# Kernel tuning notes

Hardware: AMD Instinct MI355X
Metric: run time of the kernel (lower is better)

## Reference

```python
import jax, jax.numpy as jnp
import numpy as np


def setup_inputs() -> dict:
    key = jax.random.key(0)
    k1, k2, k3, k4, k5 = jax.random.split(key, 5)
    B, S, D_IN, D_OUT = 4, 2048, 4096, 4096
    inp = jax.random.normal(k1, (B, S, D_IN), dtype=jnp.float32)
    w_q = jax.random.randint(k2, (D_OUT, D_IN), 0, 255, dtype=jnp.int32)
    scale = jax.random.uniform(k3, (D_OUT, 1), dtype=jnp.float32) * 0.02 + 1e-3
    zero_point = jax.random.randint(k4, (D_OUT, 1), 0, 255, dtype=jnp.int32)
    bias = jax.random.normal(k5, (D_OUT,), dtype=jnp.float32)
    return {"input": inp, "w_q": w_q, "scale": scale, "zero_point": zero_point, "bias": bias}


def reference(input, w_q, scale, zero_point, bias):
    # decompress_module: dequantize int weight with per-output-channel affine params
    # W[o, i] = (w_q[o, i] - zp[o]) * scale[o]   -> full fp32 weight materialized
    W = (w_q - zero_point).astype(jnp.float32) * scale  # [D_OUT, D_IN]
    # F.linear: y = x @ W^T + b
    return jnp.einsum("bsi,oi->bso", input, W) + bias
```

## Files before the change

kernel.cpp:

```cpp
#include <hip/hip_runtime.h>
#include <hip/hip_bf16.h>
#include <stdint.h>

typedef float  f32x4  __attribute__((ext_vector_type(4)));
typedef float  f32x16 __attribute__((ext_vector_type(16)));
typedef unsigned int   u32x4 __attribute__((ext_vector_type(4)));
typedef unsigned short u16x4 __attribute__((ext_vector_type(4)));
typedef int    i32x4  __attribute__((ext_vector_type(4)));

__device__ inline unsigned short f2bf(float f) {
  unsigned int u = __builtin_bit_cast(unsigned int, f);
  u += 0x7fffu + ((u >> 16) & 1u);
  return (unsigned short)(u >> 16);
}

__device__ inline void mfma32x32x16bf16(f32x16& acc, u32x4 a, u32x4 b) {
  asm volatile("v_mfma_f32_32x32x16_bf16 %0, %1, %2, %0"
               : "+v"(acc)
               : "v"(a), "v"(b));
}

__device__ inline void mfma16x16x32bf16(f32x4& acc, u32x4 a, u32x4 b) {
  asm volatile("v_mfma_f32_16x16x32_bf16 %0, %1, %2, %0"
               : "+v"(acc)
               : "v"(a), "v"(b));
}

__device__ inline void gload16(const unsigned short* src, char* ldsdst) {
  __builtin_amdgcn_global_load_lds(
      (const __attribute__((address_space(1))) void*)src,
      (__attribute__((address_space(3))) void*)ldsdst, 16, 0, 0);
}


__global__ __launch_bounds__(256) void prep_x(const float* __restrict__ x,
                                              unsigned short* __restrict__ xb,
                                              int K, int KT) {
  const int rb = blockIdx.x / KT;
  const int kt = blockIdx.x % KT;
  __shared__ unsigned short t[256 * 64];
  const int tid = threadIdx.x;
  const int klane = tid & 15;
  const int rbase = tid >> 4;
  const float* src = x + (size_t)(rb * 256) * K + kt * 64;
  const int gw = klane >> 1, hw = klane & 1;
  for (int it = 0; it < 16; ++it) {
    int row = it * 16 + rbase;
    f32x4 v = *(const f32x4*)(src + (size_t)row * K + klane * 4);
    u16x4 h;
    h[0] = f2bf(v[0]); h[1] = f2bf(v[1]); h[2] = f2bf(v[2]); h[3] = f2bf(v[3]);
    *(u16x4*)&t[row * 64 + ((gw ^ (row & 7)) << 3) + hw * 4] = h;
  }
  __syncthreads();
  unsigned short* dst = xb + ((size_t)rb * KT + kt) * 16384;
  for (int j = 0; j < 8; ++j) {
    int c = j * 256 + tid;
    int l = c & 63, f = (c >> 6) & 7, s = c >> 9;
    int row = f * 32 + (l & 31);
    int g   = (s * 2 + (l >> 5)) ^ (row & 7);
    u32x4 v = *(const u32x4*)&t[row * 64 + (g << 3)];
    *(u32x4*)(dst + (size_t)c * 8) = v;
  }
}

__global__ __launch_bounds__(256) void prep_w(const int* __restrict__ wq,
                                              const int* __restrict__ zp,
                                              unsigned short* __restrict__ wb,
                                              int K, int KT) {
  const int cb = blockIdx.x / KT;
  const int kt = blockIdx.x % KT;
  __shared__ unsigned short t[256 * 64];
  const int tid = threadIdx.x;
  const int klane = tid & 15;
  const int rbase = tid >> 4;
  const int* src = wq + (size_t)(cb * 256) * K + kt * 64;
  const int gw = klane >> 1, hw = klane & 1;
  for (int it = 0; it < 16; ++it) {
    int row = it * 16 + rbase;
    i32x4 v = *(const i32x4*)(src + (size_t)row * K + klane * 4);
    int z = zp[cb * 256 + row];
    u16x4 h;
    h[0] = f2bf((float)(v[0] - z)); h[1] = f2bf((float)(v[1] - z));
    h[2] = f2bf((float)(v[2] - z)); h[3] = f2bf((float)(v[3] - z));
    *(u16x4*)&t[row * 64 + ((gw ^ (row & 7)) << 3) + hw * 4] = h;
  }
  __syncthreads();
  unsigned short* dst = wb + ((size_t)cb * KT + kt) * 16384;
  for (int j = 0; j < 8; ++j) {
    int c = j * 256 + tid;
    int l = c & 63, f = (c >> 6) & 7, s = c >> 9;
    int row = f * 32 + (l & 31);
    int g   = (s * 2 + (l >> 5)) ^ (row & 7);
    u32x4 v = *(const u32x4*)&t[row * 64 + (g << 3)];
    *(u32x4*)(dst + (size_t)c * 8) = v;
  }
}

__global__ __launch_bounds__(512, 2) void gemm_ring(
    const unsigned short* __restrict__ xb, const unsigned short* __restrict__ wb,
    const float* __restrict__ scale, const float* __restrict__ bias,
    float* __restrict__ out, int N, int KT) {

  __shared__ unsigned short lds[65536];

  const int NB = N >> 8;
  const int nwg = gridDim.x;
  const int wg  = (blockIdx.x & 7) * (nwg >> 3) + (blockIdx.x >> 3);
  const int rb = wg / NB;
  const int cb = wg % NB;

  const int tid  = threadIdx.x;
  const int lane = tid & 63;
  const int wave = tid >> 6;
  const int wr = wave >> 2;
  const int wc = wave & 3;
  const int wr4 = wr * 4, wc2 = wc * 2;
  const int lane16 = lane * 16;

  const unsigned short* xtb = xb + (size_t)rb * (KT >> 1) * 16384;
  const unsigned short* wtb = wb + (size_t)cb * (KT >> 1) * 16384;

  f32x16 acc[4][2] = {};

  auto STAGE = [&](int u) {
    const int slot = (u & 3) << 15;
    const unsigned short* as = xtb + (size_t)u * 8192;
    const unsigned short* bs = wtb + (size_t)u * 8192;
    char* da = (char*)lds + slot + wave * 2048;
    char* db = (char*)lds + slot + 16384 + wave * 2048;
    gload16(as + wave * 1024 + lane * 8, da);
    gload16(as + wave * 1024 + 512 + lane * 8, da + 1024);
    gload16(bs + wave * 1024 + lane * 8, db);
    gload16(bs + wave * 1024 + 512 + lane * 8, db + 1024);
  };

  auto LDA = [&](int slotb, int s, int m) -> u32x4 {
    return *(const u32x4*)((const char*)lds + slotb + s * 8192 +
                           (wr4 + m) * 1024 + lane16);
  };
  auto LDB = [&](int slotb, int s, int n) -> u32x4 {
    return *(const u32x4*)((const char*)lds + slotb + 16384 + s * 8192 +
                           (wc2 + n) * 1024 + lane16);
  };

#define BODY(U, VM, ST)                                                        \
  {                                                                            \
    const int u_ = (U);                                                        \
    const int sb = (u_ & 3) << 15;                                             \
    asm volatile("s_waitcnt vmcnt(" #VM ")" ::: "memory");                     \
    __builtin_amdgcn_s_barrier();    \
                              \
    {                                                                          \
      u32x4 b0 = LDB(sb, 0, 0), b1 = LDB(sb, 0, 1);                            \
      u32x4 a0 = LDA(sb, 0, 0), a1 = LDA(sb, 0, 1);                            \
      u32x4 a2 = LDA(sb, 0, 2), a3 = LDA(sb, 0, 3);                            \
      if (ST) STAGE(u_ + 3);                                                   \
      asm volatile("s_waitcnt lgkmcnt(0)" ::: "memory");                       \
      __builtin_amdgcn_s_setprio(1);                                           \
      mfma32x32x16bf16(acc[0][0], a0, b0);                                     \
      mfma32x32x16bf16(acc[0][1], a0, b1);                                     \
      mfma32x32x16bf16(acc[1][0], a1, b0);                                     \
      mfma32x32x16bf16(acc[1][1], a1, b1);                                     \
      mfma32x32x16bf16(acc[2][0], a2, b0);                                     \
      mfma32x32x16bf16(acc[2][1], a2, b1);                                     \
      mfma32x32x16bf16(acc[3][0], a3, b0);                                     \
      mfma32x32x16bf16(acc[3][1], a3, b1);                                     \
      __builtin_amdgcn_s_setprio(0);                                           \
    }                                                                          \
    __builtin_amdgcn_s_barrier();                      \
                              \
    {                                                                          \
      u32x4 b0 = LDB(sb, 1, 0), b1 = LDB(sb, 1, 1);                            \
      u32x4 a0 = LDA(sb, 1, 0), a1 = LDA(sb, 1, 1);                            \
      u32x4 a2 = LDA(sb, 1, 2), a3 = LDA(sb, 1, 3);                            \
      asm volatile("s_waitcnt lgkmcnt(0)" ::: "memory");                       \
      __builtin_amdgcn_s_setprio(1);                                           \
      mfma32x32x16bf16(acc[0][0], a0, b0);                                     \
      mfma32x32x16bf16(acc[0][1], a0, b1);                                     \
      mfma32x32x16bf16(acc[1][0], a1, b0);                                     \
      mfma32x32x16bf16(acc[1][1], a1, b1);                                     \
      mfma32x32x16bf16(acc[2][0], a2, b0);                                     \
      mfma32x32x16bf16(acc[2][1], a2, b1);                                     \
      mfma32x32x16bf16(acc[3][0], a3, b0);                                     \
      mfma32x32x16bf16(acc[3][1], a3, b1);                                     \
      __builtin_amdgcn_s_setprio(0);                                           \
    }                                                                          \
  }

  STAGE(0); STAGE(1); STAGE(2);

  int u = 0;
  for (; u + 3 < KT; ++u) BODY(u, 8, true);
  BODY(u, 8, false); ++u;
  BODY(u, 4, false); ++u;
  BODY(u, 0, false);
#undef BODY

  const int m0 = rb * 256 + wr * 128;
  const int n0 = cb * 256 + wc * 64;
  const int l31 = lane & 31, lhi = lane >> 5;
#pragma unroll
  for (int n = 0; n < 2; ++n) {
    const int col = n0 + n * 32 + l31;
    const float sc = scale[col];
    const float bi = bias[col];
#pragma unroll
    for (int m = 0; m < 4; ++m) {
      f32x16 v = acc[m][n];
      const int rowb = m0 + m * 32 + 4 * lhi;
#pragma unroll
      for (int q = 0; q < 4; ++q)
#pragma unroll
        for (int r = 0; r < 4; ++r)
          out[(size_t)(rowb + q * 8 + r) * N + col] = v[q * 4 + r] * sc + bi;
    }
  }
}

__global__ __launch_bounds__(256) void gemm_fallback(
    const float* __restrict__ x, const int* __restrict__ wq, const int* __restrict__ zp,
    const float* __restrict__ scale, const float* __restrict__ bias,
    float* __restrict__ out, int M, int N, int K) {

  __shared__ unsigned short Alds[128 * 32];
  __shared__ unsigned short Blds[128 * 32];

  const int tid = threadIdx.x;
  const int ntile = N / 128;
  const int m0 = (blockIdx.x / ntile) * 128, n0 = (blockIdx.x % ntile) * 128;
  const int lane = tid & 63;
  const int wave = tid >> 6;
  const int wr = wave >> 1, wc = wave & 1;
  const int lr = lane & 15, lhi = lane >> 4;
  f32x4 acc[4][4] = {};
  const int ar = tid >> 3, ac4 = tid & 7;

  for (int k0 = 0; k0 < K; k0 += 32) {
#pragma unroll
    for (int p = 0; p < 4; ++p) {
      int r = p * 32 + ar;
      i32x4 w = *(const i32x4*)(wq + (size_t)(n0 + r) * K + k0 + ac4 * 4);
      int z = zp[n0 + r];
      u16x4 h;
      h[0] = f2bf((float)(w[0] - z)); h[1] = f2bf((float)(w[1] - z));
      h[2] = f2bf((float)(w[2] - z)); h[3] = f2bf((float)(w[3] - z));
      *(u16x4*)&Blds[r * 32 + ac4 * 4] = h;
    }
#pragma unroll
    for (int p = 0; p < 4; ++p) {
      int r = p * 32 + ar;
      f32x4 v = *(const f32x4*)(x + (size_t)(m0 + r) * K + k0 + ac4 * 4);
      u16x4 h;
      h[0] = f2bf(v[0]); h[1] = f2bf(v[1]); h[2] = f2bf(v[2]); h[3] = f2bf(v[3]);
      *(u16x4*)&Alds[r * 32 + ac4 * 4] = h;
    }
    __syncthreads();
    u32x4 af[4], bf[4];
#pragma unroll
    for (int i = 0; i < 4; ++i) {
      af[i] = *(const u32x4*)&Alds[(wr * 64 + i * 16 + lr) * 32 + lhi * 8];
      bf[i] = *(const u32x4*)&Blds[(wc * 64 + i * 16 + lr) * 32 + lhi * 8];
    }
#pragma unroll
    for (int i = 0; i < 4; ++i)
#pragma unroll
      for (int j = 0; j < 4; ++j)
        mfma16x16x32bf16(acc[i][j], af[i], bf[j]);
    __syncthreads();
  }
  const int crow0 = m0 + wr * 64;
  const int ccol0 = n0 + wc * 64 + lr;
#pragma unroll
  for (int j = 0; j < 4; ++j) {
    int col = ccol0 + j * 16;
    float sc = scale[col], bi = bias[col];
#pragma unroll
    for (int i = 0; i < 4; ++i) {
      int row = crow0 + i * 16 + lhi * 4;
      f32x4 v = acc[i][j];
#pragma unroll
      for (int r = 0; r < 4; ++r)
        out[(size_t)(row + r) * N + col] = v[r] * sc + bi;
    }
  }
}

extern "C" void kernel_launch(void* const* d_in, const int* in_sizes, int n_in,
                              void* d_out, int out_size, void* d_ws, size_t ws_size,
                              hipStream_t stream) {
  const float* x     = (const float*)d_in[0];
  const int*   wq    = (const int*)d_in[1];
  const float* scale = (const float*)d_in[2];
  const int*   zp    = (const int*)d_in[3];
  const float* bias  = (const float*)d_in[4];
  float* out = (float*)d_out;

  const int DOUT = in_sizes[4];
  const int DIN  = in_sizes[1] / DOUT;
  const int M    = in_sizes[0] / DIN;

  const size_t needX = (size_t)M * DIN * 2;
  const size_t needW = (size_t)DOUT * DIN * 2;

  const int nwg  = (M / 256) * (DOUT / 256);
  const int KT64 = DIN / 64;
  const int KT32 = DIN / 32;
  const bool shapes_ok = (M % 256 == 0) && (DOUT % 256 == 0) && (DIN % 64 == 0) &&
                         (nwg % 8 == 0) && (KT32 >= 8);

  if (shapes_ok && ws_size >= needX + needW) {
    unsigned short* xb = (unsigned short*)d_ws;
    unsigned short* wb = (unsigned short*)((char*)d_ws + needX);
    prep_x<<<(M / 256) * KT64, 256, 0, stream>>>(x, xb, DIN, KT64);
    prep_w<<<(DOUT / 256) * KT64, 256, 0, stream>>>(wq, zp, wb, DIN, KT64);
    gemm_ring<<<nwg, 512, 0, stream>>>(xb, wb, scale, bias, out, DOUT, KT32);
  } else {
    dim3 grid((M / 128) * (DOUT / 128));
    gemm_fallback<<<grid, 256, 0, stream>>>(x, wq, zp, scale, bias, out, M, DOUT, DIN);
  }
}
```

Before: 303.2 us.

## Prefetch next K-step LDS fragments into registers and drop mid-step barrier

Restructures the main GEMM loop so the first half-tile of A/B fragments for the next K step is read from LDS into persistent registers at the end of the current step. Those prefetched fragments feed the MFMAs at the start of the next step, overlapping LDS reads with matrix math. This removes the second per-step barrier and the explicit lgkmcnt waits, and tightens the vmcnt threshold so the next slot's data is resident before prefetch. The cost is extra live registers and a more delicate ordering between global-to-LDS staging and slot reuse.

```diff
diff --git a/kernel.cpp b/kernel.cpp
--- a/kernel.cpp
+++ b/kernel.cpp
@@ -121,6 +121,7 @@
   const unsigned short* wtb = wb + (size_t)cb * (KT >> 1) * 16384;
 
   f32x16 acc[4][2] = {};
+  u32x4 pa0, pa1, pa2, pa3, pb0, pb1;
 
   auto STAGE = [&](int u) {
     const int slot = (u & 3) << 15;
@@ -143,20 +144,29 @@
                            (wc2 + n) * 1024 + lane16);
   };
 
-#define BODY(U, VM, ST)                                                        \
+#define BODY(U, VM, ST, PF)                                                    \
   {                                                                            \
     const int u_ = (U);                                                        \
-    const int sb = (u_ & 3) << 15;                                             \
+    const int sb  = (u_ & 3) << 15;                                            \
+    const int sbn = ((u_ + 1) & 3) << 15;                                      \
     asm volatile("s_waitcnt vmcnt(" #VM ")" ::: "memory");                     \
-    __builtin_amdgcn_s_barrier();    \
-                              \
+    __builtin_amdgcn_s_barrier();                                              \
+    if (ST) STAGE(u_ + 3);                                                     \
+    __builtin_amdgcn_s_setprio(1);                                             \
+              \
+    mfma32x32x16bf16(acc[0][0], pa0, pb0);                                     \
+    mfma32x32x16bf16(acc[0][1], pa0, pb1);                                     \
+    mfma32x32x16bf16(acc[1][0], pa1, pb0);                                     \
+    mfma32x32x16bf16(acc[1][1], pa1, pb1);                                     \
+    mfma32x32x16bf16(acc[2][0], pa2, pb0);                                     \
+    mfma32x32x16bf16(acc[2][1], pa2, pb1);                                     \
+    mfma32x32x16bf16(acc[3][0], pa3, pb0);                                     \
+    mfma32x32x16bf16(acc[3][1], pa3, pb1);                                     \
+                   \
     {                                                                          \
-      u32x4 b0 = LDB(sb, 0, 0), b1 = LDB(sb, 0, 1);                            \
-      u32x4 a0 = LDA(sb, 0, 0), a1 = LDA(sb, 0, 1);                            \
-      u32x4 a2 = LDA(sb, 0, 2), a3 = LDA(sb, 0, 3);                            \
-      if (ST) STAGE(u_ + 3);                                                   \
-      asm volatile("s_waitcnt lgkmcnt(0)" ::: "memory");                       \
-      __builtin_amdgcn_s_setprio(1);                                           \
+      u32x4 b0 = LDB(sb, 1, 0), b1 = LDB(sb, 1, 1);                            \
+      u32x4 a0 = LDA(sb, 1, 0), a1 = LDA(sb, 1, 1);                            \
+      u32x4 a2 = LDA(sb, 1, 2), a3 = LDA(sb, 1, 3);                            \
       mfma32x32x16bf16(acc[0][0], a0, b0);                                     \
       mfma32x32x16bf16(acc[0][1], a0, b1);                                     \
       mfma32x32x16bf16(acc[1][0], a1, b0);                                     \
@@ -165,35 +175,27 @@
       mfma32x32x16bf16(acc[2][1], a2, b1);                                     \
       mfma32x32x16bf16(acc[3][0], a3, b0);                                     \
       mfma32x32x16bf16(acc[3][1], a3, b1);                                     \
-      __builtin_amdgcn_s_setprio(0);                                           \
     }                                                                          \
-    __builtin_amdgcn_s_barrier();                      \
-                              \
-    {                                                                          \
-      u32x4 b0 = LDB(sb, 1, 0), b1 = LDB(sb, 1, 1);                            \
-      u32x4 a0 = LDA(sb, 1, 0), a1 = LDA(sb, 1, 1);                            \
-      u32x4 a2 = LDA(sb, 1, 2), a3 = LDA(sb, 1, 3);                            \
-      asm volatile("s_waitcnt lgkmcnt(0)" ::: "memory");                       \
-      __builtin_amdgcn_s_setprio(1);                                           \
-      mfma32x32x16bf16(acc[0][0], a0, b0);                                     \
-      mfma32x32x16bf16(acc[0][1], a0, b1);                                     \
-      mfma32x32x16bf16(acc[1][0], a1, b0);                                     \
-      mfma32x32x16bf16(acc[1][1], a1, b1);                                     \
-      mfma32x32x16bf16(acc[2][0], a2, b0);                                     \
-      mfma32x32x16bf16(acc[2][1], a2, b1);                                     \
-      mfma32x32x16bf16(acc[3][0], a3, b0);                                     \
-      mfma32x32x16bf16(acc[3][1], a3, b1);                                     \
-      __builtin_amdgcn_s_setprio(0);                                           \
+    __builtin_amdgcn_s_setprio(0);                                             \
+    if (PF) {                                                                  \
+      pb0 = LDB(sbn, 0, 0); pb1 = LDB(sbn, 0, 1);                              \
+      pa0 = LDA(sbn, 0, 0); pa1 = LDA(sbn, 0, 1);                              \
+      pa2 = LDA(sbn, 0, 2); pa3 = LDA(sbn, 0, 3);                              \
     }                                                                          \
   }
 
   STAGE(0); STAGE(1); STAGE(2);
+  asm volatile("s_waitcnt vmcnt(8)" ::: "memory");
+  __builtin_amdgcn_s_barrier();
+  pb0 = LDB(0, 0, 0); pb1 = LDB(0, 0, 1);
+  pa0 = LDA(0, 0, 0); pa1 = LDA(0, 0, 1);
+  pa2 = LDA(0, 0, 2); pa3 = LDA(0, 0, 3);
 
   int u = 0;
-  for (; u + 3 < KT; ++u) BODY(u, 8, true);
-  BODY(u, 8, false); ++u;
-  BODY(u, 4, false); ++u;
-  BODY(u, 0, false);
+  for (; u + 3 < KT; ++u) BODY(u, 4, 1, 1);
+  BODY(u, 4, 0, 1); ++u;
+  BODY(u, 0, 0, 1); ++u;
+  BODY(u, 0, 0, 0);
 #undef BODY
 
   const int m0 = rb * 256 + wr * 128;
```

Result: no change. 299.4 us (-1.2%).
